# Optimization experiments

Hardware: AMD Instinct MI355X
Metric: run time of the kernel (lower is better)

Reference implementation:

```python
import jax, jax.numpy as jnp
import numpy as np

B, N, C = 4, 16384, 3
PRE, POST = 4096, 512      # NMS_PRE_MAXSIZE, NMS_POST_MAXSIZE
THRESH = 0.8               # NMS_THRESH
TWO_PI = 2.0 * np.pi


def setup_inputs() -> dict:
    key = jax.random.key(0)
    k1, k2, k3, k4, k5, k6 = jax.random.split(key, 6)
    # realistic lidar boxes: (x, y, z, dx, dy, dz, ry)
    xy = jax.random.uniform(k1, (B, N, 2)) * 70.0
    z = jax.random.uniform(k2, (B, N, 1)) * 4.0 - 2.0
    dims = jax.random.uniform(k3, (B, N, 3)) * 4.0 + 0.5
    ry = jax.random.uniform(k4, (B, N, 1)) * TWO_PI
    batch_box_preds = jnp.concatenate([xy, z, dims, ry], axis=-1)
    batch_cls_preds = jax.random.normal(k5, (B, N, C))
    # sampled gt boxes aligned to post-NMS rois: (x,y,z,dx,dy,dz,ry,label)
    gt_of_rois = jax.random.normal(k6, (B, POST, 8))
    return {"batch_box_preds": batch_box_preds,
            "batch_cls_preds": batch_cls_preds,
            "gt_of_rois": gt_of_rois}


def _bev_iou(boxes):
    # axis-aligned BEV IoU over (x, y, dx, dy); [M,7] -> [M,M]
    x, y, dx, dy = boxes[:, 0], boxes[:, 1], boxes[:, 3], boxes[:, 4]
    x1, x2 = x - dx * 0.5, x + dx * 0.5
    y1, y2 = y - dy * 0.5, y + dy * 0.5
    ix = jnp.maximum(jnp.minimum(x2[:, None], x2[None, :]) - jnp.maximum(x1[:, None], x1[None, :]), 0.0)
    iy = jnp.maximum(jnp.minimum(y2[:, None], y2[None, :]) - jnp.maximum(y1[:, None], y1[None, :]), 0.0)
    inter = ix * iy
    area = dx * dy
    return inter / (area[:, None] + area[None, :] - inter + 1e-6)


def _nms_single(box_preds, cls_preds):
    # torch.max(cls_preds, dim=1) -> scores + class labels
    scores = jnp.max(cls_preds, axis=-1)
    labels = jnp.argmax(cls_preds, axis=-1)
    # NMS_PRE_MAXSIZE top-k pre-filter (scores come out sorted descending)
    top_scores, idx = jax.lax.top_k(scores, PRE)
    top_boxes = box_preds[idx]           # [PRE, 7]
    top_labels = labels[idx]
    iou = _bev_iou(top_boxes)            # [PRE, PRE] memory-bound pairwise matrix

    def step(valid, _):
        has = jnp.any(valid)
        i = jnp.argmax(valid)            # first surviving box (highest score)
        nv = valid & (iou[i] <= THRESH)
        nv = nv.at[i].set(False)
        return jnp.where(has, nv, valid), (i, has)

    _, (sel, keep) = jax.lax.scan(step, jnp.ones((PRE,), bool), None, length=POST)
    keep_f = keep.astype(box_preds.dtype)
    rois = top_boxes[sel] * keep_f[:, None]          # zero-padded like new_zeros buffer
    roi_scores = top_scores[sel] * keep_f
    roi_labels = jnp.where(keep, top_labels[sel], 0) + 1  # +1 applied to padding too (faithful)
    return rois, roi_scores, roi_labels


def _canonical_transform(rois, gt):
    # assign_targets: move gt boxes into each ROI's canonical frame
    roi_center = rois[:, :, 0:3]
    roi_ry = rois[:, :, 6] % TWO_PI
    xyz = gt[:, :, 0:3] - roi_center
    heading = gt[:, :, 6] - roi_ry
    # rotate_points_along_z with angle = -roi_ry on first 3 dims
    a = -roi_ry
    c, s = jnp.cos(a), jnp.sin(a)
    nx = xyz[:, :, 0] * c - xyz[:, :, 1] * s
    ny = xyz[:, :, 0] * s + xyz[:, :, 1] * c
    h = heading % TWO_PI
    opposite = (h > np.pi * 0.5) & (h < np.pi * 1.5)
    h = jnp.where(opposite, (h + np.pi) % TWO_PI, h)
    h = jnp.where(h > np.pi, h - TWO_PI, h)
    h = jnp.clip(h, -np.pi / 2, np.pi / 2)
    return jnp.concatenate([nx[..., None], ny[..., None], xyz[:, :, 2:3],
                            gt[:, :, 3:6], h[..., None], gt[:, :, 7:8]], axis=-1)


def reference(batch_box_preds, batch_cls_preds, gt_of_rois):
    rois, roi_scores, roi_labels = jax.vmap(_nms_single)(batch_box_preds, batch_cls_preds)
    gt_of_rois_ct = _canonical_transform(rois, gt_of_rois)
    return rois, roi_scores, roi_labels, gt_of_rois_ct
```

## Files before the change

### kernel.cpp

```cpp
#include <hip/hip_runtime.h>
#include <cstdint>
#include <cstddef>

#define BB 4
#define NN 16384
#define PRE 4096
#define POST 512
#define NTRI 2080
#define ECAP 2048
#define SLICE 512
#define NSLICE 16
#define CANDTOT (SLICE * NSLICE)
#define NTC 8
#define NCH 16
#define TH_ORD 0xBF99999Au

typedef unsigned short u16;
typedef unsigned int u32;
typedef unsigned long long u64;

__device__ __forceinline__ u32 ord32(float f) {
  u32 u = __builtin_bit_cast(u32, f);
  return (u & 0x80000000u) ? ~u : (u | 0x80000000u);
}

__device__ __forceinline__ void slice_keys(const float* __restrict__ cls, int b, int sb,
                                           u64* dst , u32* wbase ,
                                           u32* cntout ) {
  const int t = threadIdx.x;
  const int n = (sb << 10) + t;
  const float* c = cls + ((size_t)(b << 14) + n) * 3;
  float s = fmaxf(fmaxf(c[0], c[1]), c[2]);
  u32 o = ord32(s);
  bool pred = o >= TH_ORD;
  u64 mask = __ballot(pred);
  int lane = t & 63, w = t >> 6;
  if (lane == 0) wbase[w] = (u32)__popcll(mask);
  u32 lpre = (u32)__popcll(mask & ((lane == 0) ? 0ull : (~0ull >> (64 - lane))));
  if (t < SLICE) dst[t] = 0ull;
  __syncthreads();
  if (t == 0) {
    u32 acc = 0;
#pragma unroll
    for (int i = 0; i < 16; ++i) { u32 v = wbase[i]; wbase[i] = acc; acc += v; }
    *cntout = acc < SLICE ? acc : SLICE;
  }
  __syncthreads();
  if (pred) {
    u32 pos = wbase[w] + lpre;
    if (pos < SLICE) dst[pos] = ((u64)o << 14) | (u64)(NN - 1 - n);
  }
  __syncthreads();
}

__global__ __launch_bounds__(1024) void keygen_kernel(const float* __restrict__ cls,
                                                      u64* __restrict__ keyg,
                                                      u32* __restrict__ kcnt,
                                                      u32* __restrict__ edgecnt) {
  __shared__ u64 sk[SLICE];
  __shared__ u32 wbase[16];
  __shared__ u32 scnt;
  const int b = blockIdx.x >> 4;
  const int sb = blockIdx.x & 15;
  const int t = threadIdx.x;
  if (blockIdx.x == 0 && t < BB) edgecnt[t] = 0u;
  slice_keys(cls, b, sb, sk, wbase, &scnt);
  if (t < SLICE) keyg[((size_t)blockIdx.x << 9) + t] = sk[t];
  if (t == 0) kcnt[blockIdx.x] = scnt;
}

__global__ __launch_bounds__(512) void rank_kernel(const u64* __restrict__ keyg,
                                                   const u32* __restrict__ kcnt,
                                                   u32* __restrict__ rankp) {
  __shared__ u64 sk[SLICE];
  const int bid = blockIdx.x;
  const int b = bid / (NTC * NCH);
  const int rem = bid % (NTC * NCH);
  const int ct = rem / NCH, kc = rem % NCH;
  const int t = threadIdx.x;
  sk[t] = keyg[((size_t)(b * NCH + kc) << 9) + t];
  const u64* cand = keyg + ((size_t)(b * NCH + 2 * ct) << 9);
  const u64 my0 = cand[t];
  const u64 my1 = cand[t + SLICE];
  __syncthreads();
  if ((__ballot(my0 != 0ull) | __ballot(my1 != 0ull)) == 0ull) return;
  const int kn = (int)((kcnt[b * NCH + kc] + 3u) & ~3u);
  u32 r0 = 0, r1 = 0;
  for (int k = 0; k < kn; k += 4) {
    u64 k0 = sk[k], k1 = sk[k + 1], k2 = sk[k + 2], k3 = sk[k + 3];
    r0 += (u32)(k0 > my0) + (u32)(k1 > my0) + (u32)(k2 > my0) + (u32)(k3 > my0);
    r1 += (u32)(k0 > my1) + (u32)(k1 > my1) + (u32)(k2 > my1) + (u32)(k3 > my1);
  }
  u32* rp = rankp + ((size_t)kc * BB + b) * CANDTOT + (ct << 10) + t;
  rp[0] = r0;
  rp[SLICE] = r1;
}

__global__ __launch_bounds__(512) void scatter_kernel(
    const float* __restrict__ box, const float* __restrict__ cls,
    const u64* __restrict__ keyg, const u32* __restrict__ rankp,
    u32* __restrict__ sidx, float4* __restrict__ bx4, float* __restrict__ ar,
    float* __restrict__ gsc, u32* __restrict__ glab) {
  const int b = blockIdx.x >> 4;
  const int sb = blockIdx.x & 15;
  const int t = threadIdx.x;
  const u64 mykey = keyg[((size_t)blockIdx.x << 9) + t];
  if (mykey == 0ull) return;
  const int slot = (sb << 9) + t;
  u32 r = 0;
#pragma unroll
  for (int kc = 0; kc < NCH; ++kc)
    r += rankp[((size_t)kc * BB + b) * CANDTOT + slot];
  if (r >= (u32)PRE) return;
  const int idx = (NN - 1) - (int)(mykey & 0x3FFFull);
  const int g = (b << 12) + (int)r;
  sidx[g] = (u32)idx;
  const float* bp = box + ((size_t)(b << 14) + idx) * 7;
  float x = bp[0], y = bp[1];
  float dx = bp[3], dy = bp[4];
  float4 v;
  v.x = x - dx * 0.5f;
  v.y = x + dx * 0.5f;
  v.z = y - dy * 0.5f;
  v.w = y + dy * 0.5f;
  bx4[g] = v;
  ar[g] = dx * dy;
  const float* cp = cls + ((size_t)(b << 14) + idx) * 3;
  float f0 = cp[0], f1 = cp[1], f2 = cp[2];
  int lab = 0;
  float best = f0;
  if (f1 > best) { best = f1; lab = 1; }
  if (f2 > best) { best = f2; lab = 2; }
  gsc[g] = best;
  glab[g] = (u32)lab;
}

__global__ __launch_bounds__(256) void pairs_kernel(const float4* __restrict__ bx4,
                                                    const float* __restrict__ ar,
                                                    u32* __restrict__ edgecnt,
                                                    u32* __restrict__ edges) {
  __shared__ float4 si4[64], sj4[64];
  __shared__ float sia[64], sja[64];
  const int bid = blockIdx.x;
  const int b = bid / NTRI;
  const int rr = bid % NTRI;
  int m = NTRI - 1 - rr;
  int q = (int)((sqrtf(8.0f * (float)m + 1.0f) - 1.0f) * 0.5f);
  while ((q + 1) * (q + 2) / 2 <= m) ++q;
  while (q * (q + 1) / 2 > m) --q;
  int p = m - q * (q + 1) / 2;
  const int ti = 63 - q, tj = 63 - q + p;
  const int tid = threadIdx.x;
  const int base = b << 12;
  if (tid < 64) {
    si4[tid] = bx4[base + ti * 64 + tid];
    sia[tid] = ar[base + ti * 64 + tid];
  } else if (tid < 128) {
    int l = tid - 64;
    sj4[l] = bx4[base + tj * 64 + l];
    sja[l] = ar[base + tj * 64 + l];
  }
  __syncthreads();
  const int i0 = (tid & 15) * 4, j0 = (tid >> 4) * 4;
  float4 A[4], Bv[4];
  float Aa[4], Ba[4];
#pragma unroll
  for (int a = 0; a < 4; ++a) { A[a] = si4[i0 + a]; Aa[a] = sia[i0 + a]; }
#pragma unroll
  for (int c = 0; c < 4; ++c) { Bv[c] = sj4[j0 + c]; Ba[c] = sja[j0 + c]; }
#pragma unroll
  for (int a = 0; a < 4; ++a) {
#pragma unroll
    for (int c = 0; c < 4; ++c) {
      const int i = ti * 64 + i0 + a;
      const int j = tj * 64 + j0 + c;
      if (j <= i) continue;
      float ix = fminf(A[a].y, Bv[c].y) - fmaxf(A[a].x, Bv[c].x);
      float iy = fminf(A[a].w, Bv[c].w) - fmaxf(A[a].z, Bv[c].z);
      if (ix > 0.0f && iy > 0.0f) {
        float inter = ix * iy;
        float denom = ((Aa[a] + Ba[c]) - inter) + 1e-6f;
        float iou = inter / denom;
        if (iou > 0.8f) {
          u32 pos = atomicAdd(&edgecnt[b], 1u);
          if (pos < ECAP) edges[(b << 11) + pos] = ((u32)i << 12) | (u32)j;
        }
      }
    }
  }
}

__global__ __launch_bounds__(256) void nms_kernel(
    const float* __restrict__ box, const float* __restrict__ gt,
    const u32* __restrict__ sidx, const float* __restrict__ gsc,
    const u32* __restrict__ glab, const u32* __restrict__ edgecnt,
    const u32* __restrict__ edges, float* __restrict__ out) {
  __shared__ u32 sedge[ECAP];
  __shared__ u32 ssort[ECAP];
  __shared__ u64 ssup[64];
  __shared__ u32 spop[65];
  __shared__ u16 ssel[POST];
  __shared__ u16 skeep[POST];
  const int b = blockIdx.x, tid = threadIdx.x;
  int E = (int)edgecnt[b];
  if (E > ECAP) E = ECAP;
  if (tid < 64) ssup[tid] = 0ull;
  for (int e = tid; e < E; e += 256) sedge[e] = edges[(b << 11) + e];
  for (int t2 = tid; t2 < POST; t2 += 256) ssel[t2] = 0;
  __syncthreads();
  for (int e = tid; e < E; e += 256) {
    u32 key = sedge[e];
    u32 r = 0;
    for (int k = 0; k < E; ++k) r += (u32)(sedge[k] < key);
    ssort[r] = key;
  }
  __syncthreads();
  if (tid == 0) {
    for (int e = 0; e < E; ++e) {
      u32 v = ssort[e];
      u32 i = v >> 12, j = v & 4095u;
      if (!((ssup[i >> 6] >> (i & 63u)) & 1ull)) ssup[j >> 6] |= (1ull << (j & 63u));
    }
  }
  __syncthreads();
  if (tid < 64) spop[tid] = (u32)__popcll(~ssup[tid]);
  __syncthreads();
  if (tid == 0) {
    u32 acc = 0;
    for (int w = 0; w < 64; ++w) { u32 v = spop[w]; spop[w] = acc; acc += v; }
    spop[64] = acc;
  }
  __syncthreads();
  const int ns = (int)spop[64];
  if (tid < 64) {
    u64 w = ~ssup[tid];
    u32 base2 = spop[tid];
    while (w) {
      int bit = __ffsll((unsigned long long)w) - 1;
      w &= w - 1;
      if (base2 >= (u32)POST) break;
      ssel[base2] = (u16)((tid << 6) + bit);
      ++base2;
    }
  }
  for (int t2 = tid; t2 < POST; t2 += 256) skeep[t2] = (t2 < ns) ? (u16)1 : (u16)0;
  __syncthreads();

  float* rois = out;
  float* rsc  = out + BB * POST * 7;
  float* rlb  = rsc + BB * POST;
  float* rct  = rlb + BB * POST;

  const float TWO_PI_F = 6.283185307179586f;
  const float PI_F = 3.14159265358979323846f;
  const float HALF_PI_F = 1.5707963267948966f;
  const float THREE_HALF_PI_F = 4.71238898038469f;

  for (int t = tid; t < POST; t += 256) {
    int i = ssel[t];
    int kp = skeep[t];
    int g = (b << 12) + i;
    u32 idx = sidx[g];
    const float* bp = box + ((size_t)(b << 14) + idx) * 7;
    float bx[7];
#pragma unroll
    for (int d = 0; d < 7; ++d) bx[d] = kp ? bp[d] : 0.0f;
    float* ro = rois + ((size_t)b * POST + t) * 7;
#pragma unroll
    for (int d = 0; d < 7; ++d) ro[d] = bx[d];
    rsc[b * POST + t] = kp ? gsc[g] : 0.0f;
    rlb[b * POST + t] = (float)((kp ? (int)glab[g] : 0) + 1);

    const float* gp = gt + ((size_t)b * POST + t) * 8;
    float g0 = gp[0], g1 = gp[1], g2 = gp[2], g6 = gp[6];
    float rr = fmodf(bx[6], TWO_PI_F);
    if (rr < 0.0f) rr += TWO_PI_F;
    float xyz0 = g0 - bx[0], xyz1 = g1 - bx[1], xyz2 = g2 - bx[2];
    float heading = g6 - rr;
    float aa = -rr;
    float cc = cosf(aa), s2 = sinf(aa);
    float nx = xyz0 * cc - xyz1 * s2;
    float ny = xyz0 * s2 + xyz1 * cc;
    float h = fmodf(heading, TWO_PI_F);
    if (h < 0.0f) h += TWO_PI_F;
    bool opp = (h > HALF_PI_F) && (h < THREE_HALF_PI_F);
    if (opp) {
      h = fmodf(h + PI_F, TWO_PI_F);
      if (h < 0.0f) h += TWO_PI_F;
    }
    if (h > PI_F) h -= TWO_PI_F;
    h = fminf(fmaxf(h, -HALF_PI_F), HALF_PI_F);

    float* co = rct + ((size_t)b * POST + t) * 8;
    co[0] = nx;
    co[1] = ny;
    co[2] = xyz2;
    co[3] = gp[3];
    co[4] = gp[4];
    co[5] = gp[5];
    co[6] = h;
    co[7] = gp[7];
  }
}

extern "C" void kernel_launch(void* const* d_in, const int* in_sizes, int n_in,
                              void* d_out, int out_size, void* d_ws, size_t ws_size,
                              hipStream_t stream) {
  const float* box = (const float*)d_in[0];
  const float* cls = (const float*)d_in[1];
  const float* gt  = (const float*)d_in[2];
  float* out = (float*)d_out;

  char* ws = (char*)d_ws;
  size_t off = 0;
  auto alloc = [&](size_t bytes) -> void* {
    void* p = ws + off;
    off += (bytes + 255) & ~(size_t)255;
    return p;
  };
  u32* rankp   = (u32*)alloc((size_t)NCH * BB * CANDTOT * 4);
  u32* edgecnt = (u32*)alloc((size_t)BB * 4);
  u32* sidx    = (u32*)alloc((size_t)BB * PRE * 4);
  float4* bx4  = (float4*)alloc((size_t)BB * PRE * 16);
  float* ar    = (float*)alloc((size_t)BB * PRE * 4);
  float* gsc   = (float*)alloc((size_t)BB * PRE * 4);
  u32* glab    = (u32*)alloc((size_t)BB * PRE * 4);
  u32* edges   = (u32*)alloc((size_t)BB * ECAP * 4);
  u64* keyg    = (u64*)alloc((size_t)BB * NSLICE * SLICE * 8);
  u32* kcnt    = (u32*)alloc((size_t)BB * NSLICE * 4);

  hipLaunchKernelGGL(keygen_kernel, dim3(BB * NSLICE), dim3(1024), 0, stream,
                     cls, keyg, kcnt, edgecnt);
  hipLaunchKernelGGL(rank_kernel, dim3(BB * NTC * NCH), dim3(512), 0, stream,
                     keyg, kcnt, rankp);
  hipLaunchKernelGGL(scatter_kernel, dim3(BB * NSLICE), dim3(512), 0, stream,
                     box, cls, keyg, rankp, sidx, bx4, ar, gsc, glab);
  hipLaunchKernelGGL(pairs_kernel, dim3(BB * NTRI), dim3(256), 0, stream,
                     bx4, ar, edgecnt, edges);
  hipLaunchKernelGGL(nms_kernel, dim3(BB), dim3(256), 0, stream,
                     box, gt, sidx, gsc, glab, edgecnt, edges, out);
}
```

Baseline: 102.6 us.

## Fuse five NMS stages into one persistent kernel with grid barriers

Merges the keygen, rank, scatter, pairwise-IoU and NMS kernels into a single persistent kernel of 512 blocks that separates stages with atomic-counter grid barriers. Keygen now has 512 threads handle two scores each, and the pairs stage loops over triangle tiles with a 4x2 per-thread micro-tile. Barrier counters and the edge counter are zeroed by a memset before launch. This removes four kernel launch gaps, but it depends on all 512 blocks being co-resident for the spin barriers and serializes the stages through global atomics.

```diff
diff --git a/kernel.cpp b/kernel.cpp
--- a/kernel.cpp
+++ b/kernel.cpp
@@ -14,6 +14,8 @@
 #define NTC 8
 #define NCH 16
 #define TH_ORD 0xBF99999Au
+#define NB 512
+#define NT 512
 
 typedef unsigned short u16;
 typedef unsigned int u32;
@@ -24,282 +26,291 @@
   return (u & 0x80000000u) ? ~u : (u | 0x80000000u);
 }
 
-__device__ __forceinline__ void slice_keys(const float* __restrict__ cls, int b, int sb,
-                                           u64* dst , u32* wbase ,
-                                           u32* cntout ) {
-  const int t = threadIdx.x;
-  const int n = (sb << 10) + t;
-  const float* c = cls + ((size_t)(b << 14) + n) * 3;
-  float s = fmaxf(fmaxf(c[0], c[1]), c[2]);
-  u32 o = ord32(s);
-  bool pred = o >= TH_ORD;
-  u64 mask = __ballot(pred);
-  int lane = t & 63, w = t >> 6;
-  if (lane == 0) wbase[w] = (u32)__popcll(mask);
-  u32 lpre = (u32)__popcll(mask & ((lane == 0) ? 0ull : (~0ull >> (64 - lane))));
-  if (t < SLICE) dst[t] = 0ull;
+__device__ __forceinline__ void gsync(u32* bar, int tid) {
   __syncthreads();
-  if (t == 0) {
-    u32 acc = 0;
-#pragma unroll
-    for (int i = 0; i < 16; ++i) { u32 v = wbase[i]; wbase[i] = acc; acc += v; }
-    *cntout = acc < SLICE ? acc : SLICE;
-  }
-  __syncthreads();
-  if (pred) {
-    u32 pos = wbase[w] + lpre;
-    if (pos < SLICE) dst[pos] = ((u64)o << 14) | (u64)(NN - 1 - n);
+  if (tid == 0) {
+    __hip_atomic_fetch_add(bar, 1u, __ATOMIC_ACQ_REL, __HIP_MEMORY_SCOPE_AGENT);
+    while (__hip_atomic_load(bar, __ATOMIC_ACQUIRE, __HIP_MEMORY_SCOPE_AGENT) < (u32)NB)
+      __builtin_amdgcn_s_sleep(2);
   }
   __syncthreads();
 }
 
-__global__ __launch_bounds__(1024) void keygen_kernel(const float* __restrict__ cls,
-                                                      u64* __restrict__ keyg,
-                                                      u32* __restrict__ kcnt,
-                                                      u32* __restrict__ edgecnt) {
+__global__ __launch_bounds__(NT, 4) void fused_kernel(
+    const float* __restrict__ box, const float* __restrict__ cls,
+    const float* __restrict__ gt, u32* __restrict__ rankp,
+    u32* __restrict__ sidx, float4* __restrict__ bx4, float* __restrict__ ar,
+    float* __restrict__ gsc, u32* __restrict__ glab, u32* __restrict__ edges,
+    u64* __restrict__ keyg, u32* __restrict__ kcnt, u32* __restrict__ barz,
+    float* __restrict__ out) {
   __shared__ u64 sk[SLICE];
   __shared__ u32 wbase[16];
   __shared__ u32 scnt;
-  const int b = blockIdx.x >> 4;
-  const int sb = blockIdx.x & 15;
-  const int t = threadIdx.x;
-  if (blockIdx.x == 0 && t < BB) edgecnt[t] = 0u;
-  slice_keys(cls, b, sb, sk, wbase, &scnt);
-  if (t < SLICE) keyg[((size_t)blockIdx.x << 9) + t] = sk[t];
-  if (t == 0) kcnt[blockIdx.x] = scnt;
-}
-
-__global__ __launch_bounds__(512) void rank_kernel(const u64* __restrict__ keyg,
-                                                   const u32* __restrict__ kcnt,
-                                                   u32* __restrict__ rankp) {
-  __shared__ u64 sk[SLICE];
-  const int bid = blockIdx.x;
-  const int b = bid / (NTC * NCH);
-  const int rem = bid % (NTC * NCH);
-  const int ct = rem / NCH, kc = rem % NCH;
-  const int t = threadIdx.x;
-  sk[t] = keyg[((size_t)(b * NCH + kc) << 9) + t];
-  const u64* cand = keyg + ((size_t)(b * NCH + 2 * ct) << 9);
-  const u64 my0 = cand[t];
-  const u64 my1 = cand[t + SLICE];
-  __syncthreads();
-  if ((__ballot(my0 != 0ull) | __ballot(my1 != 0ull)) == 0ull) return;
-  const int kn = (int)((kcnt[b * NCH + kc] + 3u) & ~3u);
-  u32 r0 = 0, r1 = 0;
-  for (int k = 0; k < kn; k += 4) {
-    u64 k0 = sk[k], k1 = sk[k + 1], k2 = sk[k + 2], k3 = sk[k + 3];
-    r0 += (u32)(k0 > my0) + (u32)(k1 > my0) + (u32)(k2 > my0) + (u32)(k3 > my0);
-    r1 += (u32)(k0 > my1) + (u32)(k1 > my1) + (u32)(k2 > my1) + (u32)(k3 > my1);
-  }
-  u32* rp = rankp + ((size_t)kc * BB + b) * CANDTOT + (ct << 10) + t;
-  rp[0] = r0;
-  rp[SLICE] = r1;
-}
-
-__global__ __launch_bounds__(512) void scatter_kernel(
-    const float* __restrict__ box, const float* __restrict__ cls,
-    const u64* __restrict__ keyg, const u32* __restrict__ rankp,
-    u32* __restrict__ sidx, float4* __restrict__ bx4, float* __restrict__ ar,
-    float* __restrict__ gsc, u32* __restrict__ glab) {
-  const int b = blockIdx.x >> 4;
-  const int sb = blockIdx.x & 15;
-  const int t = threadIdx.x;
-  const u64 mykey = keyg[((size_t)blockIdx.x << 9) + t];
-  if (mykey == 0ull) return;
-  const int slot = (sb << 9) + t;
-  u32 r = 0;
-#pragma unroll
-  for (int kc = 0; kc < NCH; ++kc)
-    r += rankp[((size_t)kc * BB + b) * CANDTOT + slot];
-  if (r >= (u32)PRE) return;
-  const int idx = (NN - 1) - (int)(mykey & 0x3FFFull);
-  const int g = (b << 12) + (int)r;
-  sidx[g] = (u32)idx;
-  const float* bp = box + ((size_t)(b << 14) + idx) * 7;
-  float x = bp[0], y = bp[1];
-  float dx = bp[3], dy = bp[4];
-  float4 v;
-  v.x = x - dx * 0.5f;
-  v.y = x + dx * 0.5f;
-  v.z = y - dy * 0.5f;
-  v.w = y + dy * 0.5f;
-  bx4[g] = v;
-  ar[g] = dx * dy;
-  const float* cp = cls + ((size_t)(b << 14) + idx) * 3;
-  float f0 = cp[0], f1 = cp[1], f2 = cp[2];
-  int lab = 0;
-  float best = f0;
-  if (f1 > best) { best = f1; lab = 1; }
-  if (f2 > best) { best = f2; lab = 2; }
-  gsc[g] = best;
-  glab[g] = (u32)lab;
-}
-
-__global__ __launch_bounds__(256) void pairs_kernel(const float4* __restrict__ bx4,
-                                                    const float* __restrict__ ar,
-                                                    u32* __restrict__ edgecnt,
-                                                    u32* __restrict__ edges) {
   __shared__ float4 si4[64], sj4[64];
   __shared__ float sia[64], sja[64];
-  const int bid = blockIdx.x;
-  const int b = bid / NTRI;
-  const int rr = bid % NTRI;
-  int m = NTRI - 1 - rr;
-  int q = (int)((sqrtf(8.0f * (float)m + 1.0f) - 1.0f) * 0.5f);
-  while ((q + 1) * (q + 2) / 2 <= m) ++q;
-  while (q * (q + 1) / 2 > m) --q;
-  int p = m - q * (q + 1) / 2;
-  const int ti = 63 - q, tj = 63 - q + p;
-  const int tid = threadIdx.x;
-  const int base = b << 12;
-  if (tid < 64) {
-    si4[tid] = bx4[base + ti * 64 + tid];
-    sia[tid] = ar[base + ti * 64 + tid];
-  } else if (tid < 128) {
-    int l = tid - 64;
-    sj4[l] = bx4[base + tj * 64 + l];
-    sja[l] = ar[base + tj * 64 + l];
-  }
-  __syncthreads();
-  const int i0 = (tid & 15) * 4, j0 = (tid >> 4) * 4;
-  float4 A[4], Bv[4];
-  float Aa[4], Ba[4];
-#pragma unroll
-  for (int a = 0; a < 4; ++a) { A[a] = si4[i0 + a]; Aa[a] = sia[i0 + a]; }
-#pragma unroll
-  for (int c = 0; c < 4; ++c) { Bv[c] = sj4[j0 + c]; Ba[c] = sja[j0 + c]; }
-#pragma unroll
-  for (int a = 0; a < 4; ++a) {
-#pragma unroll
-    for (int c = 0; c < 4; ++c) {
-      const int i = ti * 64 + i0 + a;
-      const int j = tj * 64 + j0 + c;
-      if (j <= i) continue;
-      float ix = fminf(A[a].y, Bv[c].y) - fmaxf(A[a].x, Bv[c].x);
-      float iy = fminf(A[a].w, Bv[c].w) - fmaxf(A[a].z, Bv[c].z);
-      if (ix > 0.0f && iy > 0.0f) {
-        float inter = ix * iy;
-        float denom = ((Aa[a] + Ba[c]) - inter) + 1e-6f;
-        float iou = inter / denom;
-        if (iou > 0.8f) {
-          u32 pos = atomicAdd(&edgecnt[b], 1u);
-          if (pos < ECAP) edges[(b << 11) + pos] = ((u32)i << 12) | (u32)j;
-        }
-      }
-    }
-  }
-}
-
-__global__ __launch_bounds__(256) void nms_kernel(
-    const float* __restrict__ box, const float* __restrict__ gt,
-    const u32* __restrict__ sidx, const float* __restrict__ gsc,
-    const u32* __restrict__ glab, const u32* __restrict__ edgecnt,
-    const u32* __restrict__ edges, float* __restrict__ out) {
   __shared__ u32 sedge[ECAP];
   __shared__ u32 ssort[ECAP];
   __shared__ u64 ssup[64];
   __shared__ u32 spop[65];
   __shared__ u16 ssel[POST];
   __shared__ u16 skeep[POST];
-  const int b = blockIdx.x, tid = threadIdx.x;
-  int E = (int)edgecnt[b];
-  if (E > ECAP) E = ECAP;
-  if (tid < 64) ssup[tid] = 0ull;
-  for (int e = tid; e < E; e += 256) sedge[e] = edges[(b << 11) + e];
-  for (int t2 = tid; t2 < POST; t2 += 256) ssel[t2] = 0;
-  __syncthreads();
-  for (int e = tid; e < E; e += 256) {
-    u32 key = sedge[e];
-    u32 r = 0;
-    for (int k = 0; k < E; ++k) r += (u32)(sedge[k] < key);
-    ssort[r] = key;
-  }
-  __syncthreads();
-  if (tid == 0) {
-    for (int e = 0; e < E; ++e) {
-      u32 v = ssort[e];
-      u32 i = v >> 12, j = v & 4095u;
-      if (!((ssup[i >> 6] >> (i & 63u)) & 1ull)) ssup[j >> 6] |= (1ull << (j & 63u));
-    }
-  }
-  __syncthreads();
-  if (tid < 64) spop[tid] = (u32)__popcll(~ssup[tid]);
-  __syncthreads();
-  if (tid == 0) {
-    u32 acc = 0;
-    for (int w = 0; w < 64; ++w) { u32 v = spop[w]; spop[w] = acc; acc += v; }
-    spop[64] = acc;
-  }
-  __syncthreads();
-  const int ns = (int)spop[64];
-  if (tid < 64) {
-    u64 w = ~ssup[tid];
-    u32 base2 = spop[tid];
-    while (w) {
-      int bit = __ffsll((unsigned long long)w) - 1;
-      w &= w - 1;
-      if (base2 >= (u32)POST) break;
-      ssel[base2] = (u16)((tid << 6) + bit);
-      ++base2;
-    }
-  }
-  for (int t2 = tid; t2 < POST; t2 += 256) skeep[t2] = (t2 < ns) ? (u16)1 : (u16)0;
-  __syncthreads();
-
-  float* rois = out;
-  float* rsc  = out + BB * POST * 7;
-  float* rlb  = rsc + BB * POST;
-  float* rct  = rlb + BB * POST;
-
-  const float TWO_PI_F = 6.283185307179586f;
-  const float PI_F = 3.14159265358979323846f;
-  const float HALF_PI_F = 1.5707963267948966f;
-  const float THREE_HALF_PI_F = 4.71238898038469f;
-
-  for (int t = tid; t < POST; t += 256) {
-    int i = ssel[t];
-    int kp = skeep[t];
-    int g = (b << 12) + i;
-    u32 idx = sidx[g];
-    const float* bp = box + ((size_t)(b << 14) + idx) * 7;
-    float bx[7];
-#pragma unroll
-    for (int d = 0; d < 7; ++d) bx[d] = kp ? bp[d] : 0.0f;
-    float* ro = rois + ((size_t)b * POST + t) * 7;
-#pragma unroll
-    for (int d = 0; d < 7; ++d) ro[d] = bx[d];
-    rsc[b * POST + t] = kp ? gsc[g] : 0.0f;
-    rlb[b * POST + t] = (float)((kp ? (int)glab[g] : 0) + 1);
-
-    const float* gp = gt + ((size_t)b * POST + t) * 8;
-    float g0 = gp[0], g1 = gp[1], g2 = gp[2], g6 = gp[6];
-    float rr = fmodf(bx[6], TWO_PI_F);
-    if (rr < 0.0f) rr += TWO_PI_F;
-    float xyz0 = g0 - bx[0], xyz1 = g1 - bx[1], xyz2 = g2 - bx[2];
-    float heading = g6 - rr;
-    float aa = -rr;
-    float cc = cosf(aa), s2 = sinf(aa);
-    float nx = xyz0 * cc - xyz1 * s2;
-    float ny = xyz0 * s2 + xyz1 * cc;
-    float h = fmodf(heading, TWO_PI_F);
-    if (h < 0.0f) h += TWO_PI_F;
-    bool opp = (h > HALF_PI_F) && (h < THREE_HALF_PI_F);
-    if (opp) {
-      h = fmodf(h + PI_F, TWO_PI_F);
+
+  const int bid = blockIdx.x;
+  const int t = threadIdx.x;
+  u32* bar = barz;
+  u32* edgecnt = barz + 8;
+
+  if (bid < BB * NSLICE) {
+    const int b = bid >> 4, sb = bid & 15;
+    const int n0 = (sb << 10) + t;
+    const int n1 = n0 + 512;
+    const float* c0 = cls + ((size_t)(b << 14) + n0) * 3;
+    const float* c1 = cls + ((size_t)(b << 14) + n1) * 3;
+    float s0 = fmaxf(fmaxf(c0[0], c0[1]), c0[2]);
+    float s1 = fmaxf(fmaxf(c1[0], c1[1]), c1[2]);
+    u32 o0 = ord32(s0), o1 = ord32(s1);
+    bool p0 = o0 >= TH_ORD, p1 = o1 >= TH_ORD;
+    u64 m0 = __ballot(p0);
+    u64 m1 = __ballot(p1);
+    int lane = t & 63, w = t >> 6;
+    if (lane == 0) { wbase[w] = (u32)__popcll(m0); wbase[8 + w] = (u32)__popcll(m1); }
+    u64 lm = (lane == 0) ? 0ull : (~0ull >> (64 - lane));
+    u32 lp0 = (u32)__popcll(m0 & lm), lp1 = (u32)__popcll(m1 & lm);
+    sk[t] = 0ull;
+    __syncthreads();
+    if (t == 0) {
+      u32 acc = 0;
+#pragma unroll
+      for (int i = 0; i < 16; ++i) { u32 v = wbase[i]; wbase[i] = acc; acc += v; }
+      scnt = acc < SLICE ? acc : SLICE;
+    }
+    __syncthreads();
+    if (p0) {
+      u32 pos = wbase[w] + lp0;
+      if (pos < SLICE) sk[pos] = ((u64)o0 << 14) | (u64)(NN - 1 - n0);
+    }
+    if (p1) {
+      u32 pos = wbase[8 + w] + lp1;
+      if (pos < SLICE) sk[pos] = ((u64)o1 << 14) | (u64)(NN - 1 - n1);
+    }
+    __syncthreads();
+    keyg[((size_t)bid << 9) + t] = sk[t];
+    if (t == 0) kcnt[bid] = scnt;
+  }
+  gsync(bar + 0, t);
+
+  {
+    const int b = bid / (NTC * NCH);
+    const int rem = bid % (NTC * NCH);
+    const int ct = rem / NCH, kc = rem % NCH;
+    sk[t] = keyg[((size_t)(b * NCH + kc) << 9) + t];
+    const u64* cand = keyg + ((size_t)(b * NCH + 2 * ct) << 9);
+    const u64 my0 = cand[t];
+    const u64 my1 = cand[t + SLICE];
+    __syncthreads();
+    if ((__ballot(my0 != 0ull) | __ballot(my1 != 0ull)) != 0ull) {
+      const int kn = (int)((kcnt[b * NCH + kc] + 3u) & ~3u);
+      u32 r0 = 0, r1 = 0;
+      for (int k = 0; k < kn; k += 4) {
+        u64 k0 = sk[k], k1 = sk[k + 1], k2 = sk[k + 2], k3 = sk[k + 3];
+        r0 += (u32)(k0 > my0) + (u32)(k1 > my0) + (u32)(k2 > my0) + (u32)(k3 > my0);
+        r1 += (u32)(k0 > my1) + (u32)(k1 > my1) + (u32)(k2 > my1) + (u32)(k3 > my1);
+      }
+      u32* rp = rankp + ((size_t)kc * BB + b) * CANDTOT + (ct << 10) + t;
+      rp[0] = r0;
+      rp[SLICE] = r1;
+    }
+  }
+  gsync(bar + 1, t);
+
+  if (bid < BB * NSLICE) {
+    const int b = bid >> 4, sb = bid & 15;
+    const u64 mykey = keyg[((size_t)bid << 9) + t];
+    if (mykey != 0ull) {
+      const int slot = (sb << 9) + t;
+      u32 r = 0;
+#pragma unroll
+      for (int kc = 0; kc < NCH; ++kc)
+        r += rankp[((size_t)kc * BB + b) * CANDTOT + slot];
+      if (r < (u32)PRE) {
+        const int idx = (NN - 1) - (int)(mykey & 0x3FFFull);
+        const int g = (b << 12) + (int)r;
+        sidx[g] = (u32)idx;
+        const float* bp = box + ((size_t)(b << 14) + idx) * 7;
+        float x = bp[0], y = bp[1];
+        float dx = bp[3], dy = bp[4];
+        float4 v;
+        v.x = x - dx * 0.5f;
+        v.y = x + dx * 0.5f;
+        v.z = y - dy * 0.5f;
+        v.w = y + dy * 0.5f;
+        bx4[g] = v;
+        ar[g] = dx * dy;
+        const float* cp = cls + ((size_t)(b << 14) + idx) * 3;
+        float f0 = cp[0], f1 = cp[1], f2 = cp[2];
+        int lab = 0;
+        float best = f0;
+        if (f1 > best) { best = f1; lab = 1; }
+        if (f2 > best) { best = f2; lab = 2; }
+        gsc[g] = best;
+        glab[g] = (u32)lab;
+      }
+    }
+  }
+  gsync(bar + 2, t);
+
+  for (int task = bid; task < BB * NTRI; task += NB) {
+    const int b = task / NTRI;
+    const int rr = task % NTRI;
+    int m = NTRI - 1 - rr;
+    int q = (int)((sqrtf(8.0f * (float)m + 1.0f) - 1.0f) * 0.5f);
+    while ((q + 1) * (q + 2) / 2 <= m) ++q;
+    while (q * (q + 1) / 2 > m) --q;
+    int p = m - q * (q + 1) / 2;
+    const int ti = 63 - q, tj = 63 - q + p;
+    const int base = b << 12;
+    __syncthreads();
+    if (t < 64) {
+      si4[t] = bx4[base + ti * 64 + t];
+      sia[t] = ar[base + ti * 64 + t];
+    } else if (t < 128) {
+      int l = t - 64;
+      sj4[l] = bx4[base + tj * 64 + l];
+      sja[l] = ar[base + tj * 64 + l];
+    }
+    __syncthreads();
+    const int i0 = (t & 15) * 4, j0 = (t >> 4) * 2;
+    float4 A[4], Bv[2];
+    float Aa[4], Ba[2];
+#pragma unroll
+    for (int a = 0; a < 4; ++a) { A[a] = si4[i0 + a]; Aa[a] = sia[i0 + a]; }
+#pragma unroll
+    for (int c = 0; c < 2; ++c) { Bv[c] = sj4[j0 + c]; Ba[c] = sja[j0 + c]; }
+#pragma unroll
+    for (int a = 0; a < 4; ++a) {
+#pragma unroll
+      for (int c = 0; c < 2; ++c) {
+        const int i = ti * 64 + i0 + a;
+        const int j = tj * 64 + j0 + c;
+        if (j <= i) continue;
+        float ix = fminf(A[a].y, Bv[c].y) - fmaxf(A[a].x, Bv[c].x);
+        float iy = fminf(A[a].w, Bv[c].w) - fmaxf(A[a].z, Bv[c].z);
+        if (ix > 0.0f && iy > 0.0f) {
+          float inter = ix * iy;
+          float denom = ((Aa[a] + Ba[c]) - inter) + 1e-6f;
+          float iou = inter / denom;
+          if (iou > 0.8f) {
+            u32 pos = atomicAdd(&edgecnt[b], 1u);
+            if (pos < ECAP) edges[(b << 11) + pos] = ((u32)i << 12) | (u32)j;
+          }
+        }
+      }
+    }
+  }
+  gsync(bar + 3, t);
+
+  if (bid >= BB) return;
+  {
+    const int b = bid;
+    int E = (int)__hip_atomic_load(&edgecnt[b], __ATOMIC_RELAXED, __HIP_MEMORY_SCOPE_AGENT);
+    if (E > ECAP) E = ECAP;
+    if (t < 64) ssup[t] = 0ull;
+    for (int e = t; e < E; e += NT) sedge[e] = edges[(b << 11) + e];
+    for (int t2 = t; t2 < POST; t2 += NT) ssel[t2] = 0;
+    __syncthreads();
+    for (int e = t; e < E; e += NT) {
+      u32 key = sedge[e];
+      u32 r = 0;
+      for (int k = 0; k < E; ++k) r += (u32)(sedge[k] < key);
+      ssort[r] = key;
+    }
+    __syncthreads();
+    if (t == 0) {
+      for (int e = 0; e < E; ++e) {
+        u32 v = ssort[e];
+        u32 i = v >> 12, j = v & 4095u;
+        if (!((ssup[i >> 6] >> (i & 63u)) & 1ull)) ssup[j >> 6] |= (1ull << (j & 63u));
+      }
+    }
+    __syncthreads();
+    if (t < 64) spop[t] = (u32)__popcll(~ssup[t]);
+    __syncthreads();
+    if (t == 0) {
+      u32 acc = 0;
+      for (int w = 0; w < 64; ++w) { u32 v = spop[w]; spop[w] = acc; acc += v; }
+      spop[64] = acc;
+    }
+    __syncthreads();
+    const int ns = (int)spop[64];
+    if (t < 64) {
+      u64 w = ~ssup[t];
+      u32 base2 = spop[t];
+      while (w) {
+        int bit = __ffsll((unsigned long long)w) - 1;
+        w &= w - 1;
+        if (base2 >= (u32)POST) break;
+        ssel[base2] = (u16)((t << 6) + bit);
+        ++base2;
+      }
+    }
+    for (int t2 = t; t2 < POST; t2 += NT) skeep[t2] = (t2 < ns) ? (u16)1 : (u16)0;
+    __syncthreads();
+
+    float* rois = out;
+    float* rsc  = out + BB * POST * 7;
+    float* rlb  = rsc + BB * POST;
+    float* rct  = rlb + BB * POST;
+
+    const float TWO_PI_F = 6.283185307179586f;
+    const float PI_F = 3.14159265358979323846f;
+    const float HALF_PI_F = 1.5707963267948966f;
+    const float THREE_HALF_PI_F = 4.71238898038469f;
+
+    for (int tt = t; tt < POST; tt += NT) {
+      int i = ssel[tt];
+      int kp = skeep[tt];
+      int g = (b << 12) + i;
+      u32 idx = sidx[g];
+      const float* bp = box + ((size_t)(b << 14) + idx) * 7;
+      float bx[7];
+#pragma unroll
+      for (int d = 0; d < 7; ++d) bx[d] = kp ? bp[d] : 0.0f;
+      float* ro = rois + ((size_t)b * POST + tt) * 7;
+#pragma unroll
+      for (int d = 0; d < 7; ++d) ro[d] = bx[d];
+      rsc[b * POST + tt] = kp ? gsc[g] : 0.0f;
+      rlb[b * POST + tt] = (float)((kp ? (int)glab[g] : 0) + 1);
+
+      const float* gp = gt + ((size_t)b * POST + tt) * 8;
+      float g0 = gp[0], g1 = gp[1], g2 = gp[2], g6 = gp[6];
+      float rr2 = fmodf(bx[6], TWO_PI_F);
+      if (rr2 < 0.0f) rr2 += TWO_PI_F;
+      float xyz0 = g0 - bx[0], xyz1 = g1 - bx[1], xyz2 = g2 - bx[2];
+      float heading = g6 - rr2;
+      float aa = -rr2;
+      float cc = cosf(aa), s2 = sinf(aa);
+      float nx = xyz0 * cc - xyz1 * s2;
+      float ny = xyz0 * s2 + xyz1 * cc;
+      float h = fmodf(heading, TWO_PI_F);
       if (h < 0.0f) h += TWO_PI_F;
-    }
-    if (h > PI_F) h -= TWO_PI_F;
-    h = fminf(fmaxf(h, -HALF_PI_F), HALF_PI_F);
-
-    float* co = rct + ((size_t)b * POST + t) * 8;
-    co[0] = nx;
-    co[1] = ny;
-    co[2] = xyz2;
-    co[3] = gp[3];
-    co[4] = gp[4];
-    co[5] = gp[5];
-    co[6] = h;
-    co[7] = gp[7];
+      bool opp = (h > HALF_PI_F) && (h < THREE_HALF_PI_F);
+      if (opp) {
+        h = fmodf(h + PI_F, TWO_PI_F);
+        if (h < 0.0f) h += TWO_PI_F;
+      }
+      if (h > PI_F) h -= TWO_PI_F;
+      h = fminf(fmaxf(h, -HALF_PI_F), HALF_PI_F);
+
+      float* co = rct + ((size_t)b * POST + tt) * 8;
+      co[0] = nx;
+      co[1] = ny;
+      co[2] = xyz2;
+      co[3] = gp[3];
+      co[4] = gp[4];
+      co[5] = gp[5];
+      co[6] = h;
+      co[7] = gp[7];
+    }
   }
 }
 
@@ -319,7 +330,6 @@
     return p;
   };
   u32* rankp   = (u32*)alloc((size_t)NCH * BB * CANDTOT * 4);
-  u32* edgecnt = (u32*)alloc((size_t)BB * 4);
   u32* sidx    = (u32*)alloc((size_t)BB * PRE * 4);
   float4* bx4  = (float4*)alloc((size_t)BB * PRE * 16);
   float* ar    = (float*)alloc((size_t)BB * PRE * 4);
@@ -328,15 +338,10 @@
   u32* edges   = (u32*)alloc((size_t)BB * ECAP * 4);
   u64* keyg    = (u64*)alloc((size_t)BB * NSLICE * SLICE * 8);
   u32* kcnt    = (u32*)alloc((size_t)BB * NSLICE * 4);
-
-  hipLaunchKernelGGL(keygen_kernel, dim3(BB * NSLICE), dim3(1024), 0, stream,
-                     cls, keyg, kcnt, edgecnt);
-  hipLaunchKernelGGL(rank_kernel, dim3(BB * NTC * NCH), dim3(512), 0, stream,
-                     keyg, kcnt, rankp);
-  hipLaunchKernelGGL(scatter_kernel, dim3(BB * NSLICE), dim3(512), 0, stream,
-                     box, cls, keyg, rankp, sidx, bx4, ar, gsc, glab);
-  hipLaunchKernelGGL(pairs_kernel, dim3(BB * NTRI), dim3(256), 0, stream,
-                     bx4, ar, edgecnt, edges);
-  hipLaunchKernelGGL(nms_kernel, dim3(BB), dim3(256), 0, stream,
-                     box, gt, sidx, gsc, glab, edgecnt, edges, out);
+  u32* barz    = (u32*)alloc(256);
+
+  hipMemsetAsync(barz, 0, 64, stream);
+  hipLaunchKernelGGL(fused_kernel, dim3(NB), dim3(NT), 0, stream,
+                     box, cls, gt, rankp, sidx, bx4, ar, gsc, glab, edges,
+                     keyg, kcnt, barz, out);
 }
```

Result: slower. 268.8 us (+162.1%).

## Replace pairwise rank with histogram bucket ranking and fuse NMS via last-block tree

Applied to the files above, without the earlier changes.

Drops the O(N^2)-style pairwise rank kernel. Keys are now bucketed into a 2048-bin histogram during keygen, and each key's rank comes from a suffix scan plus a comparison within its own bucket. The pairs and NMS kernels are merged: a hierarchical atomic counter tree lets the last finishing block per batch run the sequential NMS, and a memset replaces the in-kernel counter reset. This saves two launches and the rank work, but adds atomics, a 64-per-bucket cap that could lose correctness on skewed scores, and larger per-block shared memory in the pairs kernel, which may lower occupancy.

```diff
diff --git a/kernel.cpp b/kernel.cpp
--- a/kernel.cpp
+++ b/kernel.cpp
@@ -10,10 +10,17 @@
 #define ECAP 2048
 #define SLICE 512
 #define NSLICE 16
-#define CANDTOT (SLICE * NSLICE)
-#define NTC 8
-#define NCH 16
 #define TH_ORD 0xBF99999Au
+#define HISTB 2048
+#define HPAD 32
+#define BCAP 64
+#define DT1(b, k) (((b)*260 + (k)) * 64)
+#define DT2(b, k) (66560 + ((b)*33 + (k)) * 64)
+#define DT3(b, k) (75008 + ((b)*5 + (k)) * 64)
+#define DT4(b)    (76288 + (b)*64)
+#define ECNTL(b)  (76544 + (b)*64)
+#define BARU32 76800
+#define ARENAB ((BARU32 + BB * HISTB * HPAD) * 4)
 
 typedef unsigned short u16;
 typedef unsigned int u32;
@@ -22,6 +29,16 @@
 __device__ __forceinline__ u32 ord32(float f) {
   u32 u = __builtin_bit_cast(u32, f);
   return (u & 0x80000000u) ? ~u : (u | 0x80000000u);
+}
+
+__device__ __forceinline__ void gstore32(u32* p, u32 v) {
+  __hip_atomic_store(p, v, __ATOMIC_RELAXED, __HIP_MEMORY_SCOPE_AGENT);
+}
+__device__ __forceinline__ u32 gload32(const u32* p) {
+  return __hip_atomic_load((u32*)p, __ATOMIC_RELAXED, __HIP_MEMORY_SCOPE_AGENT);
+}
+__device__ __forceinline__ u32 gadd32(u32* p) {
+  return __hip_atomic_fetch_add(p, 1u, __ATOMIC_RELAXED, __HIP_MEMORY_SCOPE_AGENT);
 }
 
 __device__ __forceinline__ void slice_keys(const float* __restrict__ cls, int b, int sb,
@@ -55,62 +72,69 @@
 
 __global__ __launch_bounds__(1024) void keygen_kernel(const float* __restrict__ cls,
                                                       u64* __restrict__ keyg,
-                                                      u32* __restrict__ kcnt,
-                                                      u32* __restrict__ edgecnt) {
+                                                      u64* __restrict__ bkeys,
+                                                      u32* __restrict__ hist) {
   __shared__ u64 sk[SLICE];
   __shared__ u32 wbase[16];
   __shared__ u32 scnt;
   const int b = blockIdx.x >> 4;
   const int sb = blockIdx.x & 15;
   const int t = threadIdx.x;
-  if (blockIdx.x == 0 && t < BB) edgecnt[t] = 0u;
   slice_keys(cls, b, sb, sk, wbase, &scnt);
-  if (t < SLICE) keyg[((size_t)blockIdx.x << 9) + t] = sk[t];
-  if (t == 0) kcnt[blockIdx.x] = scnt;
-}
-
-__global__ __launch_bounds__(512) void rank_kernel(const u64* __restrict__ keyg,
-                                                   const u32* __restrict__ kcnt,
-                                                   u32* __restrict__ rankp) {
-  __shared__ u64 sk[SLICE];
-  const int bid = blockIdx.x;
-  const int b = bid / (NTC * NCH);
-  const int rem = bid % (NTC * NCH);
-  const int ct = rem / NCH, kc = rem % NCH;
+  if (t < SLICE) {
+    const u64 kk = sk[t];
+    keyg[((size_t)blockIdx.x << 9) + t] = kk;
+    if (kk != 0ull) {
+      u32 o = (u32)(kk >> 14);
+      u32 bkt = (o - TH_ORD) >> 13;
+      if (bkt > (u32)(HISTB - 1)) bkt = HISTB - 1;
+      u32 slot = atomicAdd(&hist[((b << 11) + bkt) * HPAD], 1u);
+      if (slot < (u32)BCAP)
+        bkeys[(((size_t)(b << 11) + bkt) << 6) + slot] = kk;
+    }
+  }
+}
+
+__global__ __launch_bounds__(512) void rankscatter_kernel(
+    const float* __restrict__ box, const float* __restrict__ cls,
+    const u64* __restrict__ keyg, const u64* __restrict__ bkeys,
+    const u32* __restrict__ hist, u32* __restrict__ sidx,
+    float4* __restrict__ bx4, float* __restrict__ ar,
+    float* __restrict__ gsc, u32* __restrict__ glab) {
+  __shared__ u32 sscan[512];
+  __shared__ u32 shist[HISTB];
+  const int b = blockIdx.x >> 4;
   const int t = threadIdx.x;
-  sk[t] = keyg[((size_t)(b * NCH + kc) << 9) + t];
-  const u64* cand = keyg + ((size_t)(b * NCH + 2 * ct) << 9);
-  const u64 my0 = cand[t];
-  const u64 my1 = cand[t + SLICE];
-  __syncthreads();
-  if ((__ballot(my0 != 0ull) | __ballot(my1 != 0ull)) == 0ull) return;
-  const int kn = (int)((kcnt[b * NCH + kc] + 3u) & ~3u);
-  u32 r0 = 0, r1 = 0;
-  for (int k = 0; k < kn; k += 4) {
-    u64 k0 = sk[k], k1 = sk[k + 1], k2 = sk[k + 2], k3 = sk[k + 3];
-    r0 += (u32)(k0 > my0) + (u32)(k1 > my0) + (u32)(k2 > my0) + (u32)(k3 > my0);
-    r1 += (u32)(k0 > my1) + (u32)(k1 > my1) + (u32)(k2 > my1) + (u32)(k3 > my1);
-  }
-  u32* rp = rankp + ((size_t)kc * BB + b) * CANDTOT + (ct << 10) + t;
-  rp[0] = r0;
-  rp[SLICE] = r1;
-}
-
-__global__ __launch_bounds__(512) void scatter_kernel(
-    const float* __restrict__ box, const float* __restrict__ cls,
-    const u64* __restrict__ keyg, const u32* __restrict__ rankp,
-    u32* __restrict__ sidx, float4* __restrict__ bx4, float* __restrict__ ar,
-    float* __restrict__ gsc, u32* __restrict__ glab) {
-  const int b = blockIdx.x >> 4;
-  const int sb = blockIdx.x & 15;
-  const int t = threadIdx.x;
+  const u32 b4 = (u32)(t << 2);
+  u32 h0 = hist[((b << 11) + b4 + 0) * HPAD];
+  u32 h1 = hist[((b << 11) + b4 + 1) * HPAD];
+  u32 h2 = hist[((b << 11) + b4 + 2) * HPAD];
+  u32 h3 = hist[((b << 11) + b4 + 3) * HPAD];
+  u32 s = h0 + h1 + h2 + h3;
+  sscan[t] = s;
+  __syncthreads();
+  for (int off = 1; off < 512; off <<= 1) {
+    u32 v = (t + off < 512) ? sscan[t + off] : 0u;
+    __syncthreads();
+    sscan[t] += v;
+    __syncthreads();
+  }
+  const u32 suf = sscan[t] - s;
+  shist[b4 + 0] = suf + h1 + h2 + h3;
+  shist[b4 + 1] = suf + h2 + h3;
+  shist[b4 + 2] = suf + h3;
+  shist[b4 + 3] = suf;
+  __syncthreads();
   const u64 mykey = keyg[((size_t)blockIdx.x << 9) + t];
   if (mykey == 0ull) return;
-  const int slot = (sb << 9) + t;
-  u32 r = 0;
-#pragma unroll
-  for (int kc = 0; kc < NCH; ++kc)
-    r += rankp[((size_t)kc * BB + b) * CANDTOT + slot];
+  u32 o = (u32)(mykey >> 14);
+  u32 bkt = (o - TH_ORD) >> 13;
+  if (bkt > (u32)(HISTB - 1)) bkt = HISTB - 1;
+  u32 r = shist[bkt];
+  u32 nb = hist[((b << 11) + bkt) * HPAD];
+  if (nb > (u32)BCAP) nb = BCAP;
+  const u64* bp2 = &bkeys[(((size_t)(b << 11) + bkt) << 6)];
+  for (u32 k2 = 0; k2 < nb; ++k2) r += (u32)(bp2[k2] > mykey);
   if (r >= (u32)PRE) return;
   const int idx = (NN - 1) - (int)(mykey & 0x3FFFull);
   const int g = (b << 12) + (int)r;
@@ -135,22 +159,33 @@
   glab[g] = (u32)lab;
 }
 
-__global__ __launch_bounds__(256) void pairs_kernel(const float4* __restrict__ bx4,
-                                                    const float* __restrict__ ar,
-                                                    u32* __restrict__ edgecnt,
-                                                    u32* __restrict__ edges) {
+__global__ __launch_bounds__(256) void pairs_nms_kernel(
+    const float4* __restrict__ bx4, const float* __restrict__ ar,
+    const float* __restrict__ box, const float* __restrict__ gt,
+    const u32* __restrict__ sidx, const float* __restrict__ gsc,
+    const u32* __restrict__ glab, u32* __restrict__ edges,
+    u32* __restrict__ arena, float* __restrict__ out) {
   __shared__ float4 si4[64], sj4[64];
   __shared__ float sia[64], sja[64];
+  __shared__ u32 sedge[ECAP];
+  __shared__ u32 ssort[ECAP];
+  __shared__ u64 ssup[64];
+  __shared__ u32 spop[65];
+  __shared__ u16 ssel[POST];
+  __shared__ u16 skeep[POST];
+  __shared__ u32 samE;
+
   const int bid = blockIdx.x;
   const int b = bid / NTRI;
   const int rr = bid % NTRI;
+  const int tid = threadIdx.x;
+  u32* edgecnt = &arena[ECNTL(b)];
   int m = NTRI - 1 - rr;
   int q = (int)((sqrtf(8.0f * (float)m + 1.0f) - 1.0f) * 0.5f);
   while ((q + 1) * (q + 2) / 2 <= m) ++q;
   while (q * (q + 1) / 2 > m) --q;
   int p = m - q * (q + 1) / 2;
   const int ti = 63 - q, tj = 63 - q + p;
-  const int tid = threadIdx.x;
   const int base = b << 12;
   if (tid < 64) {
     si4[tid] = bx4[base + ti * 64 + tid];
@@ -182,30 +217,41 @@
         float denom = ((Aa[a] + Ba[c]) - inter) + 1e-6f;
         float iou = inter / denom;
         if (iou > 0.8f) {
-          u32 pos = atomicAdd(&edgecnt[b], 1u);
-          if (pos < ECAP) edges[(b << 11) + pos] = ((u32)i << 12) | (u32)j;
+          u32 pos = gadd32(edgecnt);
+          if (pos < ECAP) gstore32(&edges[(b << 11) + pos], ((u32)i << 12) | (u32)j);
         }
       }
     }
   }
-}
-
-__global__ __launch_bounds__(256) void nms_kernel(
-    const float* __restrict__ box, const float* __restrict__ gt,
-    const u32* __restrict__ sidx, const float* __restrict__ gsc,
-    const u32* __restrict__ glab, const u32* __restrict__ edgecnt,
-    const u32* __restrict__ edges, float* __restrict__ out) {
-  __shared__ u32 sedge[ECAP];
-  __shared__ u32 ssort[ECAP];
-  __shared__ u64 ssup[64];
-  __shared__ u32 spop[65];
-  __shared__ u16 ssel[POST];
-  __shared__ u16 skeep[POST];
-  const int b = blockIdx.x, tid = threadIdx.x;
-  int E = (int)edgecnt[b];
+
+  __syncthreads();
+  if (tid == 0) {
+    asm volatile("s_waitcnt vmcnt(0)" ::: "memory");
+    u32 amE = 0;
+    u32 c1 = gadd32(&arena[DT1(b, rr >> 3)]);
+    if (c1 == 7u) {
+      const int id2 = rr >> 3;
+      u32 sz2 = ((id2 >> 3) < 32) ? 8u : 4u;
+      u32 c2 = gadd32(&arena[DT2(b, id2 >> 3)]);
+      if (c2 == sz2 - 1u) {
+        const int id3 = id2 >> 3;
+        u32 sz3 = ((id3 >> 3) < 4) ? 8u : 1u;
+        u32 c3 = gadd32(&arena[DT3(b, id3 >> 3)]);
+        if (c3 == sz3 - 1u) {
+          u32 c4 = gadd32(&arena[DT4(b)]);
+          amE = (c4 == 4u) ? 1u : 0u;
+        }
+      }
+    }
+    samE = amE;
+  }
+  __syncthreads();
+  if (samE == 0u) return;
+
+  int E = (int)gload32(edgecnt);
   if (E > ECAP) E = ECAP;
   if (tid < 64) ssup[tid] = 0ull;
-  for (int e = tid; e < E; e += 256) sedge[e] = edges[(b << 11) + e];
+  for (int e = tid; e < E; e += 256) sedge[e] = gload32(&edges[(b << 11) + e]);
   for (int t2 = tid; t2 < POST; t2 += 256) ssel[t2] = 0;
   __syncthreads();
   for (int e = tid; e < E; e += 256) {
@@ -273,11 +319,11 @@
 
     const float* gp = gt + ((size_t)b * POST + t) * 8;
     float g0 = gp[0], g1 = gp[1], g2 = gp[2], g6 = gp[6];
-    float rr = fmodf(bx[6], TWO_PI_F);
-    if (rr < 0.0f) rr += TWO_PI_F;
+    float rr2 = fmodf(bx[6], TWO_PI_F);
+    if (rr2 < 0.0f) rr2 += TWO_PI_F;
     float xyz0 = g0 - bx[0], xyz1 = g1 - bx[1], xyz2 = g2 - bx[2];
-    float heading = g6 - rr;
-    float aa = -rr;
+    float heading = g6 - rr2;
+    float aa = -rr2;
     float cc = cosf(aa), s2 = sinf(aa);
     float nx = xyz0 * cc - xyz1 * s2;
     float ny = xyz0 * s2 + xyz1 * cc;
@@ -318,8 +364,6 @@
     off += (bytes + 255) & ~(size_t)255;
     return p;
   };
-  u32* rankp   = (u32*)alloc((size_t)NCH * BB * CANDTOT * 4);
-  u32* edgecnt = (u32*)alloc((size_t)BB * 4);
   u32* sidx    = (u32*)alloc((size_t)BB * PRE * 4);
   float4* bx4  = (float4*)alloc((size_t)BB * PRE * 16);
   float* ar    = (float*)alloc((size_t)BB * PRE * 4);
@@ -327,16 +371,15 @@
   u32* glab    = (u32*)alloc((size_t)BB * PRE * 4);
   u32* edges   = (u32*)alloc((size_t)BB * ECAP * 4);
   u64* keyg    = (u64*)alloc((size_t)BB * NSLICE * SLICE * 8);
-  u32* kcnt    = (u32*)alloc((size_t)BB * NSLICE * 4);
-
+  u64* bkeys   = (u64*)alloc((size_t)BB * HISTB * BCAP * 8);
+  u32* arena   = (u32*)alloc(ARENAB);
+  u32* hist    = arena + BARU32;
+
+  hipMemsetAsync(arena, 0, ARENAB, stream);
   hipLaunchKernelGGL(keygen_kernel, dim3(BB * NSLICE), dim3(1024), 0, stream,
-                     cls, keyg, kcnt, edgecnt);
-  hipLaunchKernelGGL(rank_kernel, dim3(BB * NTC * NCH), dim3(512), 0, stream,
-                     keyg, kcnt, rankp);
-  hipLaunchKernelGGL(scatter_kernel, dim3(BB * NSLICE), dim3(512), 0, stream,
-                     box, cls, keyg, rankp, sidx, bx4, ar, gsc, glab);
-  hipLaunchKernelGGL(pairs_kernel, dim3(BB * NTRI), dim3(256), 0, stream,
-                     bx4, ar, edgecnt, edges);
-  hipLaunchKernelGGL(nms_kernel, dim3(BB), dim3(256), 0, stream,
-                     box, gt, sidx, gsc, glab, edgecnt, edges, out);
-}
+                     cls, keyg, bkeys, hist);
+  hipLaunchKernelGGL(rankscatter_kernel, dim3(BB * NSLICE), dim3(512), 0, stream,
+                     box, cls, keyg, bkeys, hist, sidx, bx4, ar, gsc, glab);
+  hipLaunchKernelGGL(pairs_nms_kernel, dim3(BB * NTRI), dim3(256), 0, stream,
+                     bx4, ar, box, gt, sidx, gsc, glab, edges, arena, out);
+}
```

After: 104.2 us. Within noise of the previous version (+1.6%).
